# Optimization experiments

Measured on AMD Instinct MI355X. Metric: run time of the kernel, lower is better.

The kernel has to match this reference:

```python
import jax, jax.numpy as jnp
import numpy as np

B, N, E = 8, 10000, 160000
D_IN, D_H = 128, 128
EPS = 1e-5


def setup_inputs() -> dict:
    key = jax.random.key(0)
    ks = jax.random.split(key, 10)
    x = jax.random.normal(ks[0], (B, N, D_IN), dtype=jnp.float32)
    h_prev = jax.random.normal(ks[1], (B, N, D_H), dtype=jnp.float32)
    edge_index = jax.random.randint(ks[2], (2, E), 0, N, dtype=jnp.int32)
    d_cat = D_IN + D_H
    s = 1.0 / np.sqrt(d_cat)
    def w(k):
        return jax.random.uniform(k, (d_cat, D_H), jnp.float32, -s, s)
    def b(k):
        return jax.random.uniform(k, (D_H,), jnp.float32, -s, s)
    return {
        "x": x, "edge_index": edge_index, "h_prev": h_prev,
        "Wz": w(ks[3]), "bz": b(ks[4]),
        "Wr": w(ks[5]), "br": b(ks[6]),
        "Wc": w(ks[7]), "bc": b(ks[8]),
        "gamma": jnp.ones((D_H,), jnp.float32),
        "beta": jnp.zeros((D_H,), jnp.float32),
    }


def _gcn(x, W, bias, src, dst, norm, n_nodes):
    # PyG GCNConv: linear transform, gather from src, weight by sym-norm, scatter-add to dst
    msg = (x @ W)[src] * norm[:, None]          # [E_total, D_H]
    return jax.ops.segment_sum(msg, dst, num_segments=n_nodes) + bias


def reference(x, edge_index, h_prev, Wz, bz, Wr, br, Wc, bc, gamma, beta):
    Bx, Nx, _ = x.shape
    BN = Bx * Nx
    x_flat = x.reshape(BN, -1)
    h_flat = h_prev.reshape(BN, -1)

    # batch the edge index with per-graph node offsets (all edges are in-range)
    offsets = (jnp.arange(Bx, dtype=edge_index.dtype) * Nx)[:, None]
    src = (edge_index[0][None, :] + offsets).reshape(-1)
    dst = (edge_index[1][None, :] + offsets).reshape(-1)

    # GCN self-loops + symmetric normalization (shared by all three convs)
    loops = jnp.arange(BN, dtype=src.dtype)
    src = jnp.concatenate([src, loops])
    dst = jnp.concatenate([dst, loops])
    deg = jax.ops.segment_sum(jnp.ones_like(dst, dtype=x.dtype), dst, num_segments=BN)
    dis = jnp.where(deg > 0, 1.0 / jnp.sqrt(jnp.maximum(deg, 1.0)), 0.0)
    norm = dis[src] * dis[dst]

    xh = jnp.concatenate([x_flat, h_flat], axis=1)
    z = jax.nn.sigmoid(_gcn(xh, Wz, bz, src, dst, norm, BN))
    r = jax.nn.sigmoid(_gcn(xh, Wr, br, src, dst, norm, BN))
    xrh = jnp.concatenate([x_flat, r * h_flat], axis=1)
    h_cand = jnp.tanh(_gcn(xrh, Wc, bc, src, dst, norm, BN))

    h_new = (1.0 - z) * h_flat + z * h_cand

    # LayerNorm over last dim
    mu = h_new.mean(axis=-1, keepdims=True)
    var = ((h_new - mu) ** 2).mean(axis=-1, keepdims=True)
    h_new = (h_new - mu) / jnp.sqrt(var + EPS) * gamma + beta
    return h_new.reshape(Bx, Nx, -1)
```

## Files before the change

### kernel.cpp

```cpp
#include <hip/hip_runtime.h>

#define NN 10000
#define BB 8
#define EE 160000
#define DH 128
#define LN_EPS 1e-5f

typedef unsigned short ushort_t;
typedef unsigned int uint_t;

typedef __bf16 bf16x8 __attribute__((ext_vector_type(8)));
typedef float floatx4 __attribute__((ext_vector_type(4)));
typedef float floatx2 __attribute__((ext_vector_type(2)));

__device__ __forceinline__ float b2f(uint_t u) { return __uint_as_float(u << 16); }
__device__ __forceinline__ ushort_t f2b(float f) {
    uint_t u = __float_as_uint(f);
    return (ushort_t)((u + 0x7fffu + ((u >> 16) & 1u)) >> 16);
}
__device__ __forceinline__ uint_t pack2(float lo, float hi) {
    return (uint_t)f2b(lo) | ((uint_t)f2b(hi) << 16);
}
__device__ __forceinline__ float sigm(float x) { return 1.0f / (1.0f + __expf(-x)); }
__device__ __forceinline__ float tanh_fast(float x) {
    float ex = __expf(2.0f * x);
    return 1.0f - 2.0f / (ex + 1.0f);
}

__device__ __forceinline__ floatx2 unpk(uint_t u) {
    floatx2 r;
    r.x = __uint_as_float(u << 16);
    r.y = __uint_as_float(u & 0xffff0000u);
    return r;
}
__device__ __forceinline__ void pk_fma(floatx2& a, floatx2 w, floatx2 v) {
    asm("v_pk_fma_f32 %0, %1, %2, %0" : "+v"(a) : "v"(w), "v"(v));
}
__device__ __forceinline__ void acc8p(floatx2* a, floatx2 w2, uint4 v) {
    pk_fma(a[0], w2, unpk(v.x));
    pk_fma(a[1], w2, unpk(v.y));
    pk_fma(a[2], w2, unpk(v.z));
    pk_fma(a[3], w2, unpk(v.w));
}


__global__ void count_deg(const int* __restrict__ ei, int* __restrict__ cnt) {
    int e = blockIdx.x * 256 + threadIdx.x;
    if (e < EE) atomicAdd(&cnt[ei[EE + e]], 1);
}

__global__ __launch_bounds__(256) void scan1(const int* __restrict__ cnt,
                                             int* __restrict__ offs,
                                             int* __restrict__ bsum) {
    __shared__ int s[256];
    const int t = threadIdx.x, idx = blockIdx.x * 256 + t;
    int x = (idx < NN) ? cnt[idx] : 0;
    s[t] = x;
    __syncthreads();
    for (int o = 1; o < 256; o <<= 1) {
        int v = s[t];
        int u = (t >= o) ? s[t - o] : 0;
        __syncthreads();
        s[t] = v + u;
        __syncthreads();
    }
    if (idx < NN) offs[idx] = s[t] - x;
    if (t == 255) bsum[blockIdx.x] = s[255];
}

__global__ __launch_bounds__(256) void scan3(const int* __restrict__ cnt,
                                             const int* __restrict__ bsum,
                                             int* __restrict__ offs,
                                             int* __restrict__ cursor,
                                             float* __restrict__ dis) {
    __shared__ int sb[40];
    __shared__ int pfx;
    const int t = threadIdx.x;
    if (t < 40) sb[t] = bsum[t];
    __syncthreads();
    if (t == 0) {
        int a = 0;
        for (int i = 0; i < blockIdx.x; ++i) a += sb[i];
        pfx = a;
    }
    __syncthreads();
    const int idx = blockIdx.x * 256 + t;
    if (idx < NN) {
        int off = offs[idx] + pfx;
        offs[idx] = off;
        cursor[idx] = off;
        dis[idx] = rsqrtf((float)(cnt[idx] + 1));
    }
    if (idx == 0) offs[NN] = EE;
}

__global__ void fill_csr(const int* __restrict__ ei, int* __restrict__ cursor,
                         const float* __restrict__ dis, int* __restrict__ csr_pk) {
    int e = blockIdx.x * 256 + threadIdx.x;
    if (e < EE) {
        int s = ei[e];
        int d = ei[EE + e];
        int pos = atomicAdd(&cursor[d], 1);
        csr_pk[pos] = (int)(((uint_t)f2b(dis[s]) << 16) | (uint_t)s);
    }
}


__global__ __launch_bounds__(256) void packwt_k(const float* __restrict__ x,
                                                const float* __restrict__ h,
                                                ushort_t* __restrict__ xb,
                                                ushort_t* __restrict__ hb,
                                                const float* __restrict__ Wz,
                                                const float* __restrict__ Wr,
                                                const float* __restrict__ Wc,
                                                ushort_t* __restrict__ Wt_zr,
                                                ushort_t* __restrict__ Wt_c) {
    if (blockIdx.x < 10000) {
        const size_t o = ((size_t)blockIdx.x * 256 + threadIdx.x) * 4;
        float4 vx = *(const float4*)(x + o);
        uint2 px;
        px.x = pack2(vx.x, vx.y);
        px.y = pack2(vx.z, vx.w);
        *(uint2*)(xb + o) = px;
        float4 vh = *(const float4*)(h + o);
        uint2 ph;
        ph.x = pack2(vh.x, vh.y);
        ph.y = pack2(vh.z, vh.w);
        *(uint2*)(hb + o) = ph;
    } else {
        const int col = blockIdx.x - 10000, k = threadIdx.x;
        if (col < 256) {
            float v = (col < 128) ? Wz[(size_t)k * 128 + col]
                                  : Wr[(size_t)k * 128 + col - 128];
            Wt_zr[(size_t)col * 256 + k] = f2b(v);
        } else {
            int c2 = col - 256;
            Wt_c[(size_t)c2 * 256 + k] = f2b(Wc[(size_t)k * 128 + c2]);
        }
    }
}


template <int NB>
__global__ __launch_bounds__(256) void gather16(
    const ushort_t* __restrict__ src0, const ushort_t* __restrict__ src1,
    const int* __restrict__ offs, const int* __restrict__ csr_pk,
    const float* __restrict__ dis, ushort_t* __restrict__ dst0,
    ushort_t* __restrict__ dst1) {
    const int tid = threadIdx.x, lane = tid & 63;
    const int b = blockIdx.x & 7;
    const int g = lane >> 4, il = lane & 15;
    const int ng = (blockIdx.x >> 3) * 16 + (tid >> 6) * 4 + g;
    const ushort_t* base0 = src0 + (size_t)b * NN * 128;
    const ushort_t* base1 = (NB == 2) ? (src1 + (size_t)b * NN * 128) : base0;
    const uint_t cofs = (uint_t)il * 8u;

    floatx2 a0[4], a1[4];
#pragma unroll
    for (int j = 0; j < 4; ++j) {
        a0[j] = (floatx2){0.f, 0.f};
        a1[j] = (floatx2){0.f, 0.f};
    }

    const int e0 = offs[ng], e1 = offs[ng + 1];
    const float dn = dis[ng];

    {
        const floatx2 d2 = {dn, dn};
        const uint_t off = (uint_t)ng * 128u + cofs;
        acc8p(a0, d2, *(const uint4*)(base0 + off));
        if (NB == 2) acc8p(a1, d2, *(const uint4*)(base1 + off));
    }

    int mx = e1 - e0;
    mx = max(mx, __shfl_xor(mx, 16));
    mx = max(mx, __shfl_xor(mx, 32));
    const int dmax = __builtin_amdgcn_readfirstlane(mx);
    const int pbase = (lane & 48) << 2;

    for (int ibase = 0; ibase < dmax; ibase += 16) {
        int pk = 0;
        const int pos = e0 + ibase + il;
        if (pos < e1) pk = csr_pk[pos];
        const int lim = (dmax - ibase) < 16 ? (dmax - ibase) : 16;
        int pidx = pbase;
#pragma unroll 1
        for (int i = 0; i < lim; i += 4) {
            const int p0 = __builtin_amdgcn_ds_bpermute(pidx, pk);
            const int p1 = __builtin_amdgcn_ds_bpermute(pidx + 4, pk);
            const int p2 = __builtin_amdgcn_ds_bpermute(pidx + 8, pk);
            const int p3 = __builtin_amdgcn_ds_bpermute(pidx + 12, pk);
            pidx += 16;
            const uint_t q0 = (uint_t)(p0 & 0xffff) * 128u + cofs;
            const uint_t q1 = (uint_t)(p1 & 0xffff) * 128u + cofs;
            const uint_t q2 = (uint_t)(p2 & 0xffff) * 128u + cofs;
            const uint_t q3 = (uint_t)(p3 & 0xffff) * 128u + cofs;
            uint4 v0 = *(const uint4*)(base0 + q0);
            uint4 v1 = *(const uint4*)(base0 + q1);
            uint4 v2 = *(const uint4*)(base0 + q2);
            uint4 v3 = *(const uint4*)(base0 + q3);
            uint4 u0, u1, u2, u3;
            if (NB == 2) {
                u0 = *(const uint4*)(base1 + q0);
                u1 = *(const uint4*)(base1 + q1);
                u2 = *(const uint4*)(base1 + q2);
                u3 = *(const uint4*)(base1 + q3);
            }
            const float f0 = __uint_as_float((uint_t)p0 & 0xffff0000u);
            const float f1 = __uint_as_float((uint_t)p1 & 0xffff0000u);
            const float f2 = __uint_as_float((uint_t)p2 & 0xffff0000u);
            const float f3 = __uint_as_float((uint_t)p3 & 0xffff0000u);
            const floatx2 w0 = {f0, f0}, w1 = {f1, f1}, w2 = {f2, f2}, w3 = {f3, f3};
            acc8p(a0, w0, v0);
            acc8p(a0, w1, v1);
            acc8p(a0, w2, v2);
            acc8p(a0, w3, v3);
            if (NB == 2) {
                acc8p(a1, w0, u0);
                acc8p(a1, w1, u1);
                acc8p(a1, w2, u2);
                acc8p(a1, w3, u3);
            }
        }
    }

    const size_t o = ((size_t)b * NN + ng) * 128 + cofs;
    uint4 st;
    st.x = pack2(a0[0].x * dn, a0[0].y * dn);
    st.y = pack2(a0[1].x * dn, a0[1].y * dn);
    st.z = pack2(a0[2].x * dn, a0[2].y * dn);
    st.w = pack2(a0[3].x * dn, a0[3].y * dn);
    *(uint4*)(dst0 + o) = st;
    if (NB == 2) {
        uint4 st1;
        st1.x = pack2(a1[0].x * dn, a1[0].y * dn);
        st1.y = pack2(a1[1].x * dn, a1[1].y * dn);
        st1.z = pack2(a1[2].x * dn, a1[2].y * dn);
        st1.w = pack2(a1[3].x * dn, a1[3].y * dn);
        *(uint4*)(dst1 + o) = st1;
    }
}


template <int PHASE>
__global__ __launch_bounds__(512) void gemm_k(
    const ushort_t* __restrict__ A1, const ushort_t* __restrict__ A2,
    const ushort_t* __restrict__ Wt, const float* __restrict__ bz,
    const float* __restrict__ br, const float* __restrict__ bc,
    const float* __restrict__ h_prev, const ushort_t* __restrict__ z_in,
    const float* __restrict__ gamma, const float* __restrict__ beta,
    ushort_t* __restrict__ z_out, ushort_t* __restrict__ rh_out,
    float* __restrict__ f_out) {
    __shared__ __align__(16) ushort_t As[128 * 72];
    __shared__ __align__(16) ushort_t Bs[128 * 72];
    const int tid = threadIdx.x;
    const int rb0 = blockIdx.x * 128;
    const int mode = (PHASE == 1) ? 2 : blockIdx.y;
    const int cb0 = (mode == 1) ? 128 : 0;

    const int wv = tid >> 6, lane = tid & 63;
    const int l15 = lane & 15, q = lane >> 4;
    const int sr = tid >> 2;
    const int kh = (tid & 3) * 16;

    floatx4 acc[8];
#pragma unroll
    for (int j = 0; j < 8; ++j) acc[j] = (floatx4){0.f, 0.f, 0.f, 0.f};

    uint4 pa0, pa1, pb0, pb1;
#define LOAD_AB(k0)                                                                   \
    {                                                                                 \
        const int kg = (k0) + kh;                                                     \
        const ushort_t* sA = (kg < 128)                                               \
                                 ? (A1 + (size_t)(rb0 + sr) * 128 + kg)               \
                                 : (A2 + (size_t)(rb0 + sr) * 128 + (kg - 128));      \
        pa0 = *(const uint4*)(sA);                                                    \
        pa1 = *(const uint4*)(sA + 8);                                                \
        const ushort_t* sB = Wt + (size_t)(cb0 + sr) * 256 + (k0) + kh;               \
        pb0 = *(const uint4*)(sB);                                                    \
        pb1 = *(const uint4*)(sB + 8);                                                \
    }

    LOAD_AB(0);
#pragma unroll
    for (int t = 0; t < 4; ++t) {
        if (t) __syncthreads();
        *(uint4*)(&As[sr * 72 + kh]) = pa0;
        *(uint4*)(&As[sr * 72 + kh + 8]) = pa1;
        *(uint4*)(&Bs[sr * 72 + kh]) = pb0;
        *(uint4*)(&Bs[sr * 72 + kh + 8]) = pb1;
        __syncthreads();
        if (t < 3) LOAD_AB((t + 1) * 64);
#pragma unroll
        for (int ks = 0; ks < 2; ++ks) {
            const int ko = ks * 32 + q * 8;
            bf16x8 a0 = *(const bf16x8*)&As[(wv * 16 + l15) * 72 + ko];
#pragma unroll
            for (int j = 0; j < 8; ++j) {
                bf16x8 b = *(const bf16x8*)&Bs[(j * 16 + l15) * 72 + ko];
                acc[j] = __builtin_amdgcn_mfma_f32_16x16x32_bf16(a0, b, acc[j], 0, 0, 0);
            }
        }
    }
#undef LOAD_AB

    if (mode == 0) {
        float bv[8];
#pragma unroll
        for (int j = 0; j < 8; ++j) bv[j] = bz[j * 16 + l15];
#pragma unroll
        for (int j = 0; j < 8; ++j)
#pragma unroll
            for (int v = 0; v < 4; ++v) {
                int row = rb0 + wv * 16 + q * 4 + v;
                z_out[(size_t)row * 128 + j * 16 + l15] = f2b(sigm(acc[j][v] + bv[j]));
            }
    } else if (mode == 1) {
        float bv[8];
#pragma unroll
        for (int j = 0; j < 8; ++j) bv[j] = br[j * 16 + l15];
#pragma unroll
        for (int j = 0; j < 8; ++j)
#pragma unroll
            for (int v = 0; v < 4; ++v) {
                int row = rb0 + wv * 16 + q * 4 + v;
                float r = sigm(acc[j][v] + bv[j]);
                float hh = h_prev[(size_t)row * 128 + j * 16 + l15];
                rh_out[(size_t)row * 128 + j * 16 + l15] = f2b(r * hh);
            }
    } else {
        float bv[8], gv[8], bev[8];
#pragma unroll
        for (int j = 0; j < 8; ++j) {
            bv[j] = bc[j * 16 + l15];
            gv[j] = gamma[j * 16 + l15];
            bev[j] = beta[j * 16 + l15];
        }
#pragma unroll
        for (int v = 0; v < 4; ++v) {
            const int row = rb0 + wv * 16 + q * 4 + v;
            float hn[8];
            float s = 0.f;
#pragma unroll
            for (int j = 0; j < 8; ++j) {
                float hc = tanh_fast(acc[j][v] + bv[j]);
                float zz = b2f((uint_t)z_in[(size_t)row * 128 + j * 16 + l15]);
                float hh = h_prev[(size_t)row * 128 + j * 16 + l15];
                hn[j] = (1.0f - zz) * hh + zz * hc;
                s += hn[j];
            }
#pragma unroll
            for (int o = 8; o > 0; o >>= 1) s += __shfl_xor(s, o);
            float mu = s * (1.0f / 128.0f);
            float vv = 0.f;
#pragma unroll
            for (int j = 0; j < 8; ++j) {
                float d = hn[j] - mu;
                vv += d * d;
            }
#pragma unroll
            for (int o = 8; o > 0; o >>= 1) vv += __shfl_xor(vv, o);
            float inv = rsqrtf(vv * (1.0f / 128.0f) + LN_EPS);
#pragma unroll
            for (int j = 0; j < 8; ++j)
                f_out[(size_t)row * 128 + j * 16 + l15] =
                    (hn[j] - mu) * inv * gv[j] + bev[j];
        }
    }
}


extern "C" void kernel_launch(void* const* d_in, const int* in_sizes, int n_in,
                              void* d_out, int out_size, void* d_ws, size_t ws_size,
                              hipStream_t stream) {
    const float* x = (const float*)d_in[0];
    const int* ei = (const int*)d_in[1];
    const float* h = (const float*)d_in[2];
    const float* Wz = (const float*)d_in[3];
    const float* bz = (const float*)d_in[4];
    const float* Wr = (const float*)d_in[5];
    const float* br = (const float*)d_in[6];
    const float* Wc = (const float*)d_in[7];
    const float* bcv = (const float*)d_in[8];
    const float* gamma = (const float*)d_in[9];
    const float* beta = (const float*)d_in[10];
    float* out = (float*)d_out;

    char* w = (char*)d_ws;
    int* offs = (int*)(w + 0);
    float* dis = (float*)(w + 40960);
    int* csr_pk = (int*)(w + 81920);
    ushort_t* Wt_zr = (ushort_t*)(w + 1041920);
    ushort_t* Wt_c = (ushort_t*)(w + 1172992);
    ushort_t* xb = (ushort_t*)(w + 1239040);
    ushort_t* hb = (ushort_t*)(w + 21719040);
    ushort_t* agg_x = (ushort_t*)(w + 42199040);
    ushort_t* agg_h = (ushort_t*)(w + 62679040);
    int* cnt = (int*)(w + 1239040);
    int* cursor = (int*)(w + 1280000);
    int* bsum = (int*)(w + 1320000);
    ushort_t* z_buf = xb;
    ushort_t* rh_bf = hb;
    ushort_t* agg_rh = agg_h;

    hipMemsetAsync(cnt, 0, NN * sizeof(int), stream);
    count_deg<<<EE / 256, 256, 0, stream>>>(ei, cnt);
    scan1<<<40, 256, 0, stream>>>(cnt, offs, bsum);
    scan3<<<40, 256, 0, stream>>>(cnt, bsum, offs, cursor, dis);
    fill_csr<<<EE / 256, 256, 0, stream>>>(ei, cursor, dis, csr_pk);
    packwt_k<<<10384, 256, 0, stream>>>(x, h, xb, hb, Wz, Wr, Wc, Wt_zr, Wt_c);

    gather16<2><<<(NN / 16) * 8, 256, 0, stream>>>(xb, hb, offs, csr_pk, dis,
                                                   agg_x, agg_h);
    gemm_k<0><<<dim3(80000 / 128, 2), 512, 0, stream>>>(
        agg_x, agg_h, Wt_zr, bz, br, bcv, h, (const ushort_t*)0, gamma, beta,
        z_buf, rh_bf, (float*)0);
    gather16<1><<<(NN / 16) * 8, 256, 0, stream>>>(rh_bf, (const ushort_t*)0, offs,
                                                   csr_pk, dis, agg_rh,
                                                   (ushort_t*)0);
    gemm_k<1><<<dim3(80000 / 128, 1), 512, 0, stream>>>(
        agg_x, agg_rh, Wt_c, bz, br, bcv, h, z_buf, gamma, beta,
        (ushort_t*)0, (ushort_t*)0, out);
}
```

Baseline: 291.7 us.

## Sort destination nodes by degree to balance gather wavefront work

Builds a degree histogram and a counting sort of nodes by in-degree, then has the gather kernels process nodes in that order so the four 16-lane groups in a wavefront handle nodes of similar degree. This is meant to cut divergence and idle lanes caused by uneven edge counts within a wave. It adds two small kernels, a memset and an indirection load per node, and loses spatial locality in the output writes and self-loop reads.

Measured after the change: 347.2 us. +19.0%, slower.

```diff
diff --git a/kernel.cpp b/kernel.cpp
--- a/kernel.cpp
+++ b/kernel.cpp
@@ -72,7 +72,8 @@
                                              const int* __restrict__ bsum,
                                              int* __restrict__ offs,
                                              int* __restrict__ cursor,
-                                             float* __restrict__ dis) {
+                                             float* __restrict__ dis,
+                                             int* __restrict__ hist) {
     __shared__ int sb[40];
     __shared__ int pfx;
     const int t = threadIdx.x;
@@ -89,9 +90,34 @@
         int off = offs[idx] + pfx;
         offs[idx] = off;
         cursor[idx] = off;
-        dis[idx] = rsqrtf((float)(cnt[idx] + 1));
+        int d = cnt[idx];
+        dis[idx] = rsqrtf((float)(d + 1));
+        atomicAdd(&hist[d < 63 ? d : 63], 1);
     }
     if (idx == 0) offs[NN] = EE;
+}
+
+__global__ __launch_bounds__(64) void bucket_scan(const int* __restrict__ hist,
+                                                  int* __restrict__ bcur) {
+    if (threadIdx.x == 0) {
+        int a = 0;
+        for (int i = 0; i < 64; ++i) {
+            int v = hist[i];
+            bcur[i] = a;
+            a += v;
+        }
+    }
+}
+
+__global__ __launch_bounds__(256) void order_k(const int* __restrict__ offs,
+                                               int* __restrict__ bcur,
+                                               int* __restrict__ order) {
+    int idx = blockIdx.x * 256 + threadIdx.x;
+    if (idx < NN) {
+        int d = offs[idx + 1] - offs[idx];
+        int pos = atomicAdd(&bcur[d < 63 ? d : 63], 1);
+        order[pos] = idx;
+    }
 }
 
 __global__ void fill_csr(const int* __restrict__ ei, int* __restrict__ cursor,
@@ -145,12 +171,13 @@
 __global__ __launch_bounds__(256) void gather16(
     const ushort_t* __restrict__ src0, const ushort_t* __restrict__ src1,
     const int* __restrict__ offs, const int* __restrict__ csr_pk,
-    const float* __restrict__ dis, ushort_t* __restrict__ dst0,
-    ushort_t* __restrict__ dst1) {
+    const float* __restrict__ dis, const int* __restrict__ order,
+    ushort_t* __restrict__ dst0, ushort_t* __restrict__ dst1) {
     const int tid = threadIdx.x, lane = tid & 63;
     const int b = blockIdx.x & 7;
     const int g = lane >> 4, il = lane & 15;
-    const int ng = (blockIdx.x >> 3) * 16 + (tid >> 6) * 4 + g;
+    const int slot = (blockIdx.x >> 3) * 16 + (tid >> 6) * 4 + g;
+    const int ng = order[slot];
     const ushort_t* base0 = src0 + (size_t)b * NN * 128;
     const ushort_t* base1 = (NB == 2) ? (src1 + (size_t)b * NN * 128) : base0;
     const uint_t cofs = (uint_t)il * 8u;
@@ -390,6 +417,9 @@
     int* offs = (int*)(w + 0);
     float* dis = (float*)(w + 40960);
     int* csr_pk = (int*)(w + 81920);
+    int* order = (int*)(w + 721920);
+    int* hist = (int*)(w + 765952);
+    int* bcur = (int*)(w + 766208);
     ushort_t* Wt_zr = (ushort_t*)(w + 1041920);
     ushort_t* Wt_c = (ushort_t*)(w + 1172992);
     ushort_t* xb = (ushort_t*)(w + 1239040);
@@ -404,19 +434,22 @@
     ushort_t* agg_rh = agg_h;
 
     hipMemsetAsync(cnt, 0, NN * sizeof(int), stream);
+    hipMemsetAsync(hist, 0, 64 * sizeof(int), stream);
     count_deg<<<EE / 256, 256, 0, stream>>>(ei, cnt);
     scan1<<<40, 256, 0, stream>>>(cnt, offs, bsum);
-    scan3<<<40, 256, 0, stream>>>(cnt, bsum, offs, cursor, dis);
+    scan3<<<40, 256, 0, stream>>>(cnt, bsum, offs, cursor, dis, hist);
+    bucket_scan<<<1, 64, 0, stream>>>(hist, bcur);
     fill_csr<<<EE / 256, 256, 0, stream>>>(ei, cursor, dis, csr_pk);
+    order_k<<<40, 256, 0, stream>>>(offs, bcur, order);
     packwt_k<<<10384, 256, 0, stream>>>(x, h, xb, hb, Wz, Wr, Wc, Wt_zr, Wt_c);
 
-    gather16<2><<<(NN / 16) * 8, 256, 0, stream>>>(xb, hb, offs, csr_pk, dis,
+    gather16<2><<<(NN / 16) * 8, 256, 0, stream>>>(xb, hb, offs, csr_pk, dis, order,
                                                    agg_x, agg_h);
     gemm_k<0><<<dim3(80000 / 128, 2), 512, 0, stream>>>(
         agg_x, agg_h, Wt_zr, bz, br, bcv, h, (const ushort_t*)0, gamma, beta,
         z_buf, rh_bf, (float*)0);
     gather16<1><<<(NN / 16) * 8, 256, 0, stream>>>(rh_bf, (const ushort_t*)0, offs,
-                                                   csr_pk, dis, agg_rh,
+                                                   csr_pk, dis, order, agg_rh,
                                                    (ushort_t*)0);
     gemm_k<1><<<dim3(80000 / 128, 1), 512, 0, stream>>>(
         agg_x, agg_rh, Wt_c, bz, br, bcv, h, z_buf, gamma, beta,
```

## Fuse degree counting into pack kernel and unroll gather inner loop by eight

Applied to the files above, without the earlier changes.

Merges the count_deg atomic kernel into the bf16 pack/weight-transpose kernel as extra leading blocks, removing one launch. cnt, cursor and bsum move to workspace regions that no longer alias xb. The gather inner loop becomes two fully unrolled batches of eight neighbours, so more independent loads are in flight per wave. The cost is higher register pressure in the gather kernel, which may lower occupancy.

After: 285.5 us. 2.1% less time.

```diff
diff --git a/kernel.cpp b/kernel.cpp
--- a/kernel.cpp
+++ b/kernel.cpp
@@ -43,11 +43,6 @@
     pk_fma(a[3], w2, unpk(v.w));
 }
 
-
-__global__ void count_deg(const int* __restrict__ ei, int* __restrict__ cnt) {
-    int e = blockIdx.x * 256 + threadIdx.x;
-    if (e < EE) atomicAdd(&cnt[ei[EE + e]], 1);
-}
 
 __global__ __launch_bounds__(256) void scan1(const int* __restrict__ cnt,
                                              int* __restrict__ offs,
@@ -106,17 +101,25 @@
 }
 
 
-__global__ __launch_bounds__(256) void packwt_k(const float* __restrict__ x,
-                                                const float* __restrict__ h,
-                                                ushort_t* __restrict__ xb,
-                                                ushort_t* __restrict__ hb,
-                                                const float* __restrict__ Wz,
-                                                const float* __restrict__ Wr,
-                                                const float* __restrict__ Wc,
-                                                ushort_t* __restrict__ Wt_zr,
-                                                ushort_t* __restrict__ Wt_c) {
-    if (blockIdx.x < 10000) {
-        const size_t o = ((size_t)blockIdx.x * 256 + threadIdx.x) * 4;
+__global__ __launch_bounds__(256) void cp_k(const int* __restrict__ ei,
+                                            int* __restrict__ cnt,
+                                            const float* __restrict__ x,
+                                            const float* __restrict__ h,
+                                            ushort_t* __restrict__ xb,
+                                            ushort_t* __restrict__ hb,
+                                            const float* __restrict__ Wz,
+                                            const float* __restrict__ Wr,
+                                            const float* __restrict__ Wc,
+                                            ushort_t* __restrict__ Wt_zr,
+                                            ushort_t* __restrict__ Wt_c) {
+    if (blockIdx.x < 625) {
+        int e = blockIdx.x * 256 + threadIdx.x;
+        atomicAdd(&cnt[ei[EE + e]], 1);
+        return;
+    }
+    const int bid = blockIdx.x - 625;
+    if (bid < 10000) {
+        const size_t o = ((size_t)bid * 256 + threadIdx.x) * 4;
         float4 vx = *(const float4*)(x + o);
         uint2 px;
         px.x = pack2(vx.x, vx.y);
@@ -128,7 +131,7 @@
         ph.y = pack2(vh.z, vh.w);
         *(uint2*)(hb + o) = ph;
     } else {
-        const int col = blockIdx.x - 10000, k = threadIdx.x;
+        const int col = bid - 10000, k = threadIdx.x;
         if (col < 256) {
             float v = (col < 128) ? Wz[(size_t)k * 128 + col]
                                   : Wr[(size_t)k * 128 + col - 128];
@@ -183,45 +186,33 @@
         const int pos = e0 + ibase + il;
         if (pos < e1) pk = csr_pk[pos];
         const int lim = (dmax - ibase) < 16 ? (dmax - ibase) : 16;
-        int pidx = pbase;
-#pragma unroll 1
-        for (int i = 0; i < lim; i += 4) {
-            const int p0 = __builtin_amdgcn_ds_bpermute(pidx, pk);
-            const int p1 = __builtin_amdgcn_ds_bpermute(pidx + 4, pk);
-            const int p2 = __builtin_amdgcn_ds_bpermute(pidx + 8, pk);
-            const int p3 = __builtin_amdgcn_ds_bpermute(pidx + 12, pk);
-            pidx += 16;
-            const uint_t q0 = (uint_t)(p0 & 0xffff) * 128u + cofs;
-            const uint_t q1 = (uint_t)(p1 & 0xffff) * 128u + cofs;
-            const uint_t q2 = (uint_t)(p2 & 0xffff) * 128u + cofs;
-            const uint_t q3 = (uint_t)(p3 & 0xffff) * 128u + cofs;
-            uint4 v0 = *(const uint4*)(base0 + q0);
-            uint4 v1 = *(const uint4*)(base0 + q1);
-            uint4 v2 = *(const uint4*)(base0 + q2);
-            uint4 v3 = *(const uint4*)(base0 + q3);
-            uint4 u0, u1, u2, u3;
-            if (NB == 2) {
-                u0 = *(const uint4*)(base1 + q0);
-                u1 = *(const uint4*)(base1 + q1);
-                u2 = *(const uint4*)(base1 + q2);
-                u3 = *(const uint4*)(base1 + q3);
-            }
-            const float f0 = __uint_as_float((uint_t)p0 & 0xffff0000u);
-            const float f1 = __uint_as_float((uint_t)p1 & 0xffff0000u);
-            const float f2 = __uint_as_float((uint_t)p2 & 0xffff0000u);
-            const float f3 = __uint_as_float((uint_t)p3 & 0xffff0000u);
-            const floatx2 w0 = {f0, f0}, w1 = {f1, f1}, w2 = {f2, f2}, w3 = {f3, f3};
-            acc8p(a0, w0, v0);
-            acc8p(a0, w1, v1);
-            acc8p(a0, w2, v2);
-            acc8p(a0, w3, v3);
-            if (NB == 2) {
-                acc8p(a1, w0, u0);
-                acc8p(a1, w1, u1);
-                acc8p(a1, w2, u2);
-                acc8p(a1, w3, u3);
-            }
-        }
+
+#define PROC8(OFF)                                                                   \
+    {                                                                                \
+        int p[8];                                                                    \
+        uint_t q[8];                                                                 \
+        _Pragma("unroll") for (int k = 0; k < 8; ++k) p[k] =                         \
+            __builtin_amdgcn_ds_bpermute(pbase + ((OFF) + k) * 4, pk);               \
+        _Pragma("unroll") for (int k = 0; k < 8; ++k) q[k] =                         \
+            (uint_t)(p[k] & 0xffff) * 128u + cofs;                                   \
+        uint4 v[8];                                                                  \
+        _Pragma("unroll") for (int k = 0; k < 8; ++k) v[k] =                         \
+            *(const uint4*)(base0 + q[k]);                                           \
+        uint4 u[8];                                                                  \
+        if (NB == 2) {                                                               \
+            _Pragma("unroll") for (int k = 0; k < 8; ++k) u[k] =                     \
+                *(const uint4*)(base1 + q[k]);                                       \
+        }                                                                            \
+        _Pragma("unroll") for (int k = 0; k < 8; ++k) {                              \
+            const float f = __uint_as_float((uint_t)p[k] & 0xffff0000u);             \
+            const floatx2 w2 = {f, f};                                               \
+            acc8p(a0, w2, v[k]);                                                     \
+            if (NB == 2) acc8p(a1, w2, u[k]);                                        \
+        }                                                                            \
+    }
+        PROC8(0);
+        if (lim > 8) PROC8(8);
+#undef PROC8
     }
 
     const size_t o = ((size_t)b * NN + ng) * 128 + cofs;
@@ -390,25 +381,24 @@
     int* offs = (int*)(w + 0);
     float* dis = (float*)(w + 40960);
     int* csr_pk = (int*)(w + 81920);
+    int* cnt = (int*)(w + 721920);
+    int* cursor = (int*)(w + 762880);
+    int* bsum = (int*)(w + 803840);
     ushort_t* Wt_zr = (ushort_t*)(w + 1041920);
     ushort_t* Wt_c = (ushort_t*)(w + 1172992);
     ushort_t* xb = (ushort_t*)(w + 1239040);
     ushort_t* hb = (ushort_t*)(w + 21719040);
     ushort_t* agg_x = (ushort_t*)(w + 42199040);
     ushort_t* agg_h = (ushort_t*)(w + 62679040);
-    int* cnt = (int*)(w + 1239040);
-    int* cursor = (int*)(w + 1280000);
-    int* bsum = (int*)(w + 1320000);
     ushort_t* z_buf = xb;
     ushort_t* rh_bf = hb;
     ushort_t* agg_rh = agg_h;
 
     hipMemsetAsync(cnt, 0, NN * sizeof(int), stream);
-    count_deg<<<EE / 256, 256, 0, stream>>>(ei, cnt);
+    cp_k<<<11009, 256, 0, stream>>>(ei, cnt, x, h, xb, hb, Wz, Wr, Wc, Wt_zr, Wt_c);
     scan1<<<40, 256, 0, stream>>>(cnt, offs, bsum);
     scan3<<<40, 256, 0, stream>>>(cnt, bsum, offs, cursor, dis);
     fill_csr<<<EE / 256, 256, 0, stream>>>(ei, cursor, dis, csr_pk);
-    packwt_k<<<10384, 256, 0, stream>>>(x, h, xb, hb, Wz, Wr, Wc, Wt_zr, Wt_c);
 
     gather16<2><<<(NN / 16) * 8, 256, 0, stream>>>(xb, hb, offs, csr_pk, dis,
                                                    agg_x, agg_h);
```
